# Performance work log

Hardware: AMD Instinct MI355X
Metric: run time of the kernel (lower is better)

The kernel has to match this reference:

```python
import jax, jax.numpy as jnp
import numpy as np

V, SMAX, D, L, H, F = 50257, 1024, 768, 12, 12, 3072
DH = D // H
SCALE = float(np.sqrt(DH))


def setup_inputs() -> dict:
    key = jax.random.key(0)
    ks = jax.random.split(key, 24)
    B, S = 2, 1024
    std = 0.02
    inp = {
        'input_ids': jax.random.randint(ks[0], (B, S), 0, V),
        'tok_emb': jax.random.normal(ks[1], (V, D), jnp.float32) * std,
        'pos_emb': jax.random.normal(ks[2], (SMAX, D), jnp.float32) * std,
        # stacked per-layer params (leading dim L)
        'Wq': jax.random.normal(ks[3], (L, D, D), jnp.float32) * std,
        'bq': jnp.zeros((L, D), jnp.float32),
        'Wk': jax.random.normal(ks[4], (L, D, D), jnp.float32) * std,
        'bk': jnp.zeros((L, D), jnp.float32),
        'Wv': jax.random.normal(ks[5], (L, D, D), jnp.float32) * std,
        'bv': jnp.zeros((L, D), jnp.float32),
        'Wo': jax.random.normal(ks[6], (L, D, D), jnp.float32) * std,
        'bo': jnp.zeros((L, D), jnp.float32),
        'ln1_g': jnp.ones((L, D), jnp.float32),
        'ln1_b': jnp.zeros((L, D), jnp.float32),
        'ln2_g': jnp.ones((L, D), jnp.float32),
        'ln2_b': jnp.zeros((L, D), jnp.float32),
        'W1': jax.random.normal(ks[7], (L, D, F), jnp.float32) * std,
        'b1': jnp.zeros((L, F), jnp.float32),
        'W2': jax.random.normal(ks[8], (L, F, D), jnp.float32) * std,
        'b2': jnp.zeros((L, D), jnp.float32),
        'lnf_g': jnp.ones((D,), jnp.float32),
        'lnf_b': jnp.zeros((D,), jnp.float32),
        'Whead': jax.random.normal(ks[9], (D, V), jnp.float32) * std,
    }
    return inp


def _layernorm(x, g, b, eps=1e-5):
    mu = jnp.mean(x, axis=-1, keepdims=True)
    var = jnp.var(x, axis=-1, keepdims=True)
    return (x - mu) * jax.lax.rsqrt(var + eps) * g + b


def _gpt_forward(input_ids, tok_emb, pos_emb, Wq, bq, Wk, bk, Wv, bv, Wo, bo,
                 ln1_g, ln1_b, ln2_g, ln2_b, W1, b1, W2, b2, lnf_g, lnf_b, Whead):
    B, S = input_ids.shape
    x = tok_emb[input_ids] + pos_emb[:S][None, :, :]  # (B,S,D)
    # additive causal mask: -inf above the diagonal
    idx = jnp.arange(S)
    neg_inf = jnp.finfo(x.dtype).min
    mask = jnp.where(idx[None, :] > idx[:, None], neg_inf, 0.0).astype(x.dtype)  # (S,S)

    def block(x, p):
        (wq, bq_, wk, bk_, wv, bv_, wo, bo_, g1, b1_, g2, b2_, w1, bb1, w2, bb2) = p
        h = _layernorm(x, g1, b1_)
        q = (h @ wq + bq_).reshape(B, S, H, DH)
        k = (h @ wk + bk_).reshape(B, S, H, DH)
        v = (h @ wv + bv_).reshape(B, S, H, DH)
        scores = jnp.einsum('bqhd,bkhd->bhqk', q, k) / SCALE + mask
        attn = jax.nn.softmax(scores, axis=-1)
        o = jnp.einsum('bhqk,bkhd->bqhd', attn, v).reshape(B, S, D)
        x = x + (o @ wo + bo_)
        h2 = _layernorm(x, g2, b2_)
        ffn = jax.nn.gelu(h2 @ w1 + bb1, approximate=False) @ w2 + bb2
        return x + ffn, None

    params = (Wq, bq, Wk, bk, Wv, bv, Wo, bo, ln1_g, ln1_b, ln2_g, ln2_b, W1, b1, W2, b2)
    x, _ = jax.lax.scan(block, x, params)
    x = _layernorm(x, lnf_g, lnf_b)
    return x @ Whead  # (B,S,V) logits


def reference(input_ids, tok_emb, pos_emb, Wq, bq, Wk, bk, Wv, bv, Wo, bo,
              ln1_g, ln1_b, ln2_g, ln2_b, W1, b1, W2, b2, lnf_g, lnf_b, Whead):
    return _gpt_forward(input_ids, tok_emb, pos_emb, Wq, bq, Wk, bk, Wv, bv, Wo, bo,
                        ln1_g, ln1_b, ln2_g, ln2_b, W1, b1, W2, b2, lnf_g, lnf_b, Whead)
```

## Files before the change

kernel.cpp:

```cpp
#include <hip/hip_runtime.h>
#include <hip/hip_bf16.h>
#include <cstdint>
#include <cstddef>

#define DEV __device__ __forceinline__

typedef __attribute__((ext_vector_type(8))) short short8;
typedef __attribute__((ext_vector_type(4))) short s16x4;
typedef __attribute__((ext_vector_type(4))) float f32x4;
typedef unsigned short u16;
typedef unsigned int u32;

static constexpr int Vv = 50257;
static constexpr int Dd = 768;
static constexpr int Ll = 12;
static constexpr int Hh = 12;
static constexpr int Ff = 3072;
static constexpr int Ss = 1024;
static constexpr int Bbatch = 2;
static constexpr int DHh = 64;
static constexpr int Mtok = Bbatch * Ss;
static constexpr int NQKV = 3 * Dd;
static constexpr int VPAD = 50304;

DEV u16 f2bf(float f){ u32 x; __builtin_memcpy(&x, &f, 4); x += 0x7fffu + ((x >> 16) & 1u); return (u16)(x >> 16); }

DEV void gld_lds16(const void* g, void* l){
  __builtin_amdgcn_global_load_lds((const __attribute__((address_space(1))) void*)g,
                                   (__attribute__((address_space(3))) void*)l, 16, 0, 0);
}

__global__ __launch_bounds__(256) void k_embed_ln(const int* __restrict__ ids, const float* __restrict__ tok,
                                                  const float* __restrict__ pos, const float* __restrict__ g,
                                                  const float* __restrict__ b, float* __restrict__ x,
                                                  u16* __restrict__ h){
  int t = blockIdx.x, tid = threadIdx.x;
  int id = ids[t];
  int s = t & (Ss - 1);
  const float* tr = tok + (size_t)id * Dd;
  const float* pr = pos + (size_t)s * Dd;
  float v0 = tr[tid] + pr[tid], v1 = tr[tid + 256] + pr[tid + 256], v2 = tr[tid + 512] + pr[tid + 512];
  float* xr = x + (size_t)t * Dd;
  xr[tid] = v0; xr[tid + 256] = v1; xr[tid + 512] = v2;
  float sm = v0 + v1 + v2, ss = v0 * v0 + v1 * v1 + v2 * v2;
  for (int o = 1; o < 64; o <<= 1){ sm += __shfl_xor(sm, o, 64); ss += __shfl_xor(ss, o, 64); }
  __shared__ float red[8];
  int w = tid >> 6, l = tid & 63;
  if (l == 0){ red[w] = sm; red[w + 4] = ss; }
  __syncthreads();
  sm = red[0] + red[1] + red[2] + red[3];
  ss = red[4] + red[5] + red[6] + red[7];
  float mu = sm * (1.0f / Dd);
  float var = ss * (1.0f / Dd) - mu * mu;
  float rs = rsqrtf(var + 1e-5f);
  u16* yr = h + (size_t)t * Dd;
  yr[tid]       = f2bf((v0 - mu) * rs * g[tid]       + b[tid]);
  yr[tid + 256] = f2bf((v1 - mu) * rs * g[tid + 256] + b[tid + 256]);
  yr[tid + 512] = f2bf((v2 - mu) * rs * g[tid + 512] + b[tid + 512]);
}

__global__ __launch_bounds__(256) void k_ln(const float* __restrict__ x, const float* __restrict__ g,
                                            const float* __restrict__ b, u16* __restrict__ y){
  int row = blockIdx.x, tid = threadIdx.x;
  const float* xr = x + (size_t)row * Dd;
  float v0 = xr[tid], v1 = xr[tid + 256], v2 = xr[tid + 512];
  float s = v0 + v1 + v2, ss = v0 * v0 + v1 * v1 + v2 * v2;
  for (int o = 1; o < 64; o <<= 1){ s += __shfl_xor(s, o, 64); ss += __shfl_xor(ss, o, 64); }
  __shared__ float red[8];
  int w = tid >> 6, l = tid & 63;
  if (l == 0){ red[w] = s; red[w + 4] = ss; }
  __syncthreads();
  s = red[0] + red[1] + red[2] + red[3];
  ss = red[4] + red[5] + red[6] + red[7];
  float mu = s * (1.0f / Dd);
  float var = ss * (1.0f / Dd) - mu * mu;
  float rs = rsqrtf(var + 1e-5f);
  u16* yr = y + (size_t)row * Dd;
  yr[tid]       = f2bf((v0 - mu) * rs * g[tid]       + b[tid]);
  yr[tid + 256] = f2bf((v1 - mu) * rs * g[tid + 256] + b[tid + 256]);
  yr[tid + 512] = f2bf((v2 - mu) * rs * g[tid + 512] + b[tid + 512]);
}

__global__ __launch_bounds__(256) void k_combineln(const float* __restrict__ p, const float* __restrict__ bias,
                                                   float* __restrict__ x, const float* __restrict__ g,
                                                   const float* __restrict__ b, u16* __restrict__ h){
  constexpr size_t SL = (size_t)Mtok * Dd;
  int row = blockIdx.x, tid = threadIdx.x;
  float* xr = x + (size_t)row * Dd;
  const float* p0 = p + (size_t)row * Dd;
  const float* p1 = p0 + SL;
  float v0 = xr[tid]       + p0[tid]       + p1[tid]       + bias[tid];
  float v1 = xr[tid + 256] + p0[tid + 256] + p1[tid + 256] + bias[tid + 256];
  float v2 = xr[tid + 512] + p0[tid + 512] + p1[tid + 512] + bias[tid + 512];
  xr[tid] = v0; xr[tid + 256] = v1; xr[tid + 512] = v2;
  float s = v0 + v1 + v2, ss = v0 * v0 + v1 * v1 + v2 * v2;
  for (int o = 1; o < 64; o <<= 1){ s += __shfl_xor(s, o, 64); ss += __shfl_xor(ss, o, 64); }
  __shared__ float red[8];
  int w = tid >> 6, l = tid & 63;
  if (l == 0){ red[w] = s; red[w + 4] = ss; }
  __syncthreads();
  s = red[0] + red[1] + red[2] + red[3];
  ss = red[4] + red[5] + red[6] + red[7];
  float mu = s * (1.0f / Dd);
  float var = ss * (1.0f / Dd) - mu * mu;
  float rs = rsqrtf(var + 1e-5f);
  u16* yr = h + (size_t)row * Dd;
  yr[tid]       = f2bf((v0 - mu) * rs * g[tid]       + b[tid]);
  yr[tid + 256] = f2bf((v1 - mu) * rs * g[tid + 256] + b[tid + 256]);
  yr[tid + 512] = f2bf((v2 - mu) * rs * g[tid + 512] + b[tid + 512]);
}

__global__ __launch_bounds__(256) void k_transpose(const float* __restrict__ src, u16* __restrict__ dst,
                                                   int R, int C, long smat, long dmat){
  __shared__ float tile[64][33];
  src += (size_t)blockIdx.z * smat;
  dst += (size_t)blockIdx.z * dmat;
  int c0 = blockIdx.x * 32, r0 = blockIdx.y * 64;
  int tid = threadIdx.x;
  int tc = tid & 31, tr = tid >> 5;
  #pragma unroll
  for (int i = 0; i < 8; i++){
    int r = tr + i * 8, c = c0 + tc;
    tile[r][tc] = (c < C) ? src[(size_t)(r0 + r) * C + c] : 0.0f;
  }
  __syncthreads();
  #pragma unroll
  for (int it = 0; it < 2; it++){
    int id = it * 256 + tid;
    int c = id & 31, rg = id >> 5, r = rg * 4;
    int cc = c0 + c;
    if (cc < C){
      s16x4 v = { (short)f2bf(tile[r][c]), (short)f2bf(tile[r + 1][c]),
                  (short)f2bf(tile[r + 2][c]), (short)f2bf(tile[r + 3][c]) };
      *(s16x4*)(dst + (size_t)cc * R + r0 + r) = v;
    }
  }
}

__global__ void k_biaspack(const float* __restrict__ bq, const float* __restrict__ bk,
                           const float* __restrict__ bv, float* __restrict__ o){
  int i = blockIdx.x * 256 + threadIdx.x;
  int col = i % NQKV, lay = i / NQKV;
  float v = (col < Dd) ? bq[lay * Dd + col]
          : (col < 2 * Dd) ? bk[lay * Dd + col - Dd]
          : bv[lay * Dd + col - 2 * Dd];
  o[i] = v;
}

template<int BM, int BN, int EPI>
__global__ __launch_bounds__(256) void k_gemmF(const u16* __restrict__ A, const u16* __restrict__ Bt,
    const float* __restrict__ bias, float* __restrict__ Cf, u16* __restrict__ Cb,
    u16* __restrict__ vt, int Nn, int MT, int NT){
  constexpr bool SPLIT = (EPI == 4);
  constexpr int KST  = SPLIT ? Ff : Dd;
  constexpr int KLEN = SPLIT ? (Ff / 2) : Dd;
  constexpr int nk = KLEN / 32;
  constexpr int HM = BM / 2, HN = BN / 2, FM = HM / 16, FN = HN / 16;
  constexpr int nA = (BM * 4) / 256, nB = (BN * 4) / 256;
  constexpr int ABYTE = BM * 64, BBYTE = BN * 64;
  __shared__ __align__(16) u16 ldsA[2 * BM * 32];
  __shared__ __align__(16) u16 ldsB[2 * BN * 32];
  int tid = threadIdx.x, wid = tid >> 6, l = tid & 63;
  int wm = wid >> 1, wn = wid & 1;
  int lr = l & 15, lc = l >> 4;
  int nwg = gridDim.x, dIdx = blockIdx.x;
  int L = (dIdx & 7) * (nwg >> 3) + (dIdx >> 3);
  int kidx = 0;
  if (SPLIT){ int per = MT * NT; kidx = L / per; L -= kidx * per; }
  int mtile = L % MT, ntile = L / MT;
  int m0 = mtile * BM, n0 = ntile * BN;
  int kbase = kidx * KLEN;

  const u16* gA[nA]; u16* dA[nA];
  const u16* gB[nB]; u16* dB[nB];
  #pragma unroll
  for (int i = 0; i < nA; i++){
    int id = i * 256 + tid, row = id >> 2, c = id & 3;
    int cs = c ^ ((row >> 1) & 3);
    gA[i] = A + (size_t)(m0 + row) * KST + kbase + cs * 8;
    dA[i] = ldsA + id * 8;
  }
  #pragma unroll
  for (int i = 0; i < nB; i++){
    int id = i * 256 + tid, row = id >> 2, c = id & 3;
    int cs = c ^ ((row >> 1) & 3);
    gB[i] = Bt + (size_t)(n0 + row) * KST + kbase + cs * 8;
    dB[i] = ldsB + id * 8;
  }
  int offA[FM], offB[FN];
  #pragma unroll
  for (int i = 0; i < FM; i++){
    int row = wm * HM + i * 16 + lr;
    offA[i] = row * 64 + ((lc ^ ((row >> 1) & 3)) << 4);
  }
  #pragma unroll
  for (int j = 0; j < FN; j++){
    int row = wn * HN + j * 16 + lr;
    offB[j] = row * 64 + ((lc ^ ((row >> 1) & 3)) << 4);
  }

  f32x4 acc[FM][FN];
  #pragma unroll
  for (int i = 0; i < FM; i++)
    #pragma unroll
    for (int j = 0; j < FN; j++) acc[i][j] = (f32x4)0.0f;

  auto stage = [&](int buf){
    #pragma unroll
    for (int i = 0; i < nA; i++){ gld_lds16(gA[i], (char*)dA[i] + buf * ABYTE); gA[i] += 32; }
    #pragma unroll
    for (int i = 0; i < nB; i++){ gld_lds16(gB[i], (char*)dB[i] + buf * BBYTE); gB[i] += 32; }
  };
  auto compute = [&](int buf){
    const char* bA = (const char*)ldsA + buf * ABYTE;
    const char* bB = (const char*)ldsB + buf * BBYTE;
    short8 af[FM], bfr[FN];
    #pragma unroll
    for (int i = 0; i < FM; i++) af[i] = *(const short8*)(bA + offA[i]);
    #pragma unroll
    for (int j = 0; j < FN; j++) bfr[j] = *(const short8*)(bB + offB[j]);
    #pragma unroll
    for (int i = 0; i < FM; i++)
      #pragma unroll
      for (int j = 0; j < FN; j++){
        if (EPI == 0)
          acc[i][j] = __builtin_amdgcn_mfma_f32_16x16x32_bf16(af[i], bfr[j], acc[i][j], 0, 0, 0);
        else
          acc[i][j] = __builtin_amdgcn_mfma_f32_16x16x32_bf16(bfr[j], af[i], acc[i][j], 0, 0, 0);
      }
  };

  stage(0);
  __syncthreads();
  #pragma unroll 1
  for (int t = 0; t < nk - 1; ++t){
    stage((t + 1) & 1);
    compute(t & 1);
    __syncthreads();
  }
  compute((nk - 1) & 1);

  if (EPI == 0){
    #pragma unroll
    for (int i = 0; i < FM; i++){
      #pragma unroll
      for (int j = 0; j < FN; j++){
        int col = n0 + wn * HN + j * 16 + lr;
        if (col >= Nn) continue;
        #pragma unroll
        for (int r = 0; r < 4; r++){
          int row = m0 + wm * HM + i * 16 + lc * 4 + r;
          Cf[(size_t)row * Nn + col] = acc[i][j][r];
        }
      }
    }
    return;
  }
  #pragma unroll
  for (int i = 0; i < FM; i++){
    int row = m0 + wm * HM + i * 16 + lr;
    #pragma unroll
    for (int j = 0; j < FN; j++){
      int c0 = n0 + wn * HN + j * 16 + lc * 4;
      f32x4 v = acc[i][j];
      if (EPI == 4){
        *(f32x4*)(Cf + (size_t)kidx * Mtok * Dd + (size_t)row * Dd + c0) = v;
        continue;
      }
      f32x4 bv = *(const f32x4*)(bias + c0);
      v = v + bv;
      if (EPI == 3){
        f32x4* p = (f32x4*)(Cf + (size_t)row * Nn + c0);
        *p = *p + v;
        continue;
      }
      if (EPI == 1 && c0 < Dd) v = v * 0.125f;
      if (EPI == 2){
        #pragma unroll
        for (int r = 0; r < 4; r++) v[r] = 0.5f * v[r] * (1.0f + erff(v[r] * 0.70710678118f));
      }
      u16 q0 = f2bf(v[0]), q1 = f2bf(v[1]), q2 = f2bf(v[2]), q3 = f2bf(v[3]);
      if (EPI == 1 && c0 >= 2 * Dd){
        int c2 = c0 - 2 * Dd, hh = c2 >> 6, dd2 = c2 & 63;
        int bb = row >> 10, ss2 = row & 1023;
        size_t base = ((size_t)((bb * Hh + hh) * DHh + dd2)) << 10;
        vt[base + ss2] = q0;
        vt[base + (1 << 10) + ss2] = q1;
        vt[base + (2 << 10) + ss2] = q2;
        vt[base + (3 << 10) + ss2] = q3;
      } else {
        s16x4 pv = { (short)q0, (short)q1, (short)q2, (short)q3 };
        *(s16x4*)(Cb + (size_t)row * Nn + c0) = pv;
      }
    }
  }
}

__global__ __launch_bounds__(256) void k_attn(const u16* __restrict__ qkv, const u16* __restrict__ vt,
                                              u16* __restrict__ o){
  __shared__ __align__(16) u16 ldsK[64 * 64];
  __shared__ __align__(16) u16 ldsV[64 * 64];
  __shared__ __align__(16) u16 ldsP[4][16 * 72];
  int bid = blockIdx.x;
  int iq = (Ss / 64) - 1 - (bid / (Bbatch * Hh));
  int bh = bid % (Bbatch * Hh);
  int b = bh / Hh, h = bh % Hh;
  int tid = threadIdx.x, wid = tid >> 6, l = tid & 63, lr = l & 15, lc = l >> 4;
  int nt = iq + 1;
  int qrow = b * Ss + iq * 64 + wid * 16 + lr;
  const u16* qp = qkv + (size_t)qrow * NQKV + h * DHh;
  short8 qf0 = *(const short8*)(qp + lc * 8);
  short8 qf1 = *(const short8*)(qp + 32 + lc * 8);

  const u16* gK[2]; const u16* gV[2]; u16* dK[2]; u16* dV[2];
  #pragma unroll
  for (int c = 0; c < 2; c++){
    int id = c * 256 + tid, row = id >> 3, ch = id & 7;
    int cs = ch ^ (row & 7);
    gK[c] = qkv + (size_t)(b * Ss + row) * NQKV + Dd + h * DHh + cs * 8;
    gV[c] = vt + ((size_t)(bh * DHh) + row) * Ss + cs * 8;
    dK[c] = ldsK + id * 8;
    dV[c] = ldsV + id * 8;
  }
  int koff[4][2];
  #pragma unroll
  for (int fn = 0; fn < 4; fn++){
    int kv = fn * 16 + lr;
    #pragma unroll
    for (int ks = 0; ks < 2; ks++){
      int ch = ks * 4 + lc;
      koff[fn][ks] = kv * 128 + ((ch ^ (kv & 7)) << 4);
    }
  }

  float mreg = -1e30f, lsum = 0.0f;
  f32x4 oacc[4];
  #pragma unroll
  for (int i = 0; i < 4; i++) oacc[i] = (f32x4)0.0f;
  u16* pbase = ldsP[wid];

  #pragma unroll 1
  for (int t = 0; t < nt; ++t){
    #pragma unroll
    for (int c = 0; c < 2; c++){ gld_lds16(gK[c], dK[c]); gK[c] += (size_t)64 * NQKV; }
    #pragma unroll
    for (int c = 0; c < 2; c++){ gld_lds16(gV[c], dV[c]); gV[c] += 64; }
    __syncthreads();
    f32x4 sc[4];
    __builtin_amdgcn_s_setprio(1);
    #pragma unroll
    for (int fn = 0; fn < 4; fn++){
      short8 kf0 = *(const short8*)((const char*)ldsK + koff[fn][0]);
      short8 kf1 = *(const short8*)((const char*)ldsK + koff[fn][1]);
      sc[fn] = __builtin_amdgcn_mfma_f32_16x16x32_bf16(kf0, qf0, (f32x4)0.0f, 0, 0, 0);
      sc[fn] = __builtin_amdgcn_mfma_f32_16x16x32_bf16(kf1, qf1, sc[fn], 0, 0, 0);
    }
    __builtin_amdgcn_s_setprio(0);
    if (t == iq){
      #pragma unroll
      for (int fn = 0; fn < 4; fn++)
        #pragma unroll
        for (int r = 0; r < 4; r++)
          if (fn * 16 + lc * 4 + r > wid * 16 + lr) sc[fn][r] = -1e30f;
    }
    float pm = sc[0][0];
    #pragma unroll
    for (int fn = 0; fn < 4; fn++)
      #pragma unroll
      for (int r = 0; r < 4; r++) pm = fmaxf(pm, sc[fn][r]);
    pm = fmaxf(pm, __shfl_xor(pm, 16, 64));
    pm = fmaxf(pm, __shfl_xor(pm, 32, 64));
    float mnew = fmaxf(mreg, pm);
    float alpha = __expf(mreg - mnew);
    mreg = mnew;
    float rs = 0.0f;
    #pragma unroll
    for (int fn = 0; fn < 4; fn++)
      #pragma unroll
      for (int r = 0; r < 4; r++){
        float p = __expf(sc[fn][r] - mnew);
        sc[fn][r] = p;
        rs += p;
      }
    rs += __shfl_xor(rs, 16, 64);
    rs += __shfl_xor(rs, 32, 64);
    lsum = lsum * alpha + rs;
    #pragma unroll
    for (int fn = 0; fn < 4; fn++){
      s16x4 pv = { (short)f2bf(sc[fn][0]), (short)f2bf(sc[fn][1]),
                   (short)f2bf(sc[fn][2]), (short)f2bf(sc[fn][3]) };
      *(s16x4*)((char*)pbase + lr * 144 + fn * 32 + lc * 8) = pv;
    }
    asm volatile("s_waitcnt lgkmcnt(0)" ::: "memory");
    __builtin_amdgcn_sched_barrier(0);
    #pragma unroll
    for (int fd = 0; fd < 4; fd++)
      #pragma unroll
      for (int r = 0; r < 4; r++) oacc[fd][r] *= alpha;
    short8 pa0 = *(const short8*)((const char*)pbase + lr * 144 + lc * 16);
    short8 pa1 = *(const short8*)((const char*)pbase + lr * 144 + 64 + lc * 16);
    __builtin_amdgcn_s_setprio(1);
    #pragma unroll
    for (int fd = 0; fd < 4; fd++){
      short8 vf0 = *(const short8*)((const char*)ldsV + koff[fd][0]);
      short8 vf1 = *(const short8*)((const char*)ldsV + koff[fd][1]);
      oacc[fd] = __builtin_amdgcn_mfma_f32_16x16x32_bf16(vf0, pa0, oacc[fd], 0, 0, 0);
      oacc[fd] = __builtin_amdgcn_mfma_f32_16x16x32_bf16(vf1, pa1, oacc[fd], 0, 0, 0);
    }
    __builtin_amdgcn_s_setprio(0);
    __syncthreads();
  }
  float inv = 1.0f / lsum;
  int rowg = b * Ss + iq * 64 + wid * 16 + lr;
  #pragma unroll
  for (int fd = 0; fd < 4; fd++){
    s16x4 ov = { (short)f2bf(oacc[fd][0] * inv), (short)f2bf(oacc[fd][1] * inv),
                 (short)f2bf(oacc[fd][2] * inv), (short)f2bf(oacc[fd][3] * inv) };
    *(s16x4*)(o + (size_t)rowg * Dd + h * DHh + fd * 16 + lc * 4) = ov;
  }
}

extern "C" void kernel_launch(void* const* d_in, const int* in_sizes, int n_in,
                              void* d_out, int out_size, void* d_ws, size_t ws_size,
                              hipStream_t stream){
  const int*   ids  = (const int*)d_in[0];
  const float* tok  = (const float*)d_in[1];
  const float* pos  = (const float*)d_in[2];
  const float* Wq   = (const float*)d_in[3];
  const float* bq   = (const float*)d_in[4];
  const float* Wk   = (const float*)d_in[5];
  const float* bk   = (const float*)d_in[6];
  const float* Wv   = (const float*)d_in[7];
  const float* bv   = (const float*)d_in[8];
  const float* Wo   = (const float*)d_in[9];
  const float* bo   = (const float*)d_in[10];
  const float* ln1g = (const float*)d_in[11];
  const float* ln1b = (const float*)d_in[12];
  const float* ln2g = (const float*)d_in[13];
  const float* ln2b = (const float*)d_in[14];
  const float* W1   = (const float*)d_in[15];
  const float* b1   = (const float*)d_in[16];
  const float* W2   = (const float*)d_in[17];
  const float* b2   = (const float*)d_in[18];
  const float* lnfg = (const float*)d_in[19];
  const float* lnfb = (const float*)d_in[20];
  const float* Wh   = (const float*)d_in[21];
  float* out = (float*)d_out;

  auto al = [](size_t x){ return (x + 255) & ~(size_t)255; };
  size_t off = 0;
  auto take = [&](size_t bytes){ size_t r = off; off = al(off + bytes); return r; };
  size_t o_x    = take((size_t)Mtok * Dd * 4);
  size_t o_h    = take((size_t)Mtok * Dd * 2);
  size_t o_qkv  = take((size_t)Mtok * NQKV * 2);
  size_t o_vt   = take((size_t)Bbatch * Hh * DHh * Ss * 2);
  size_t o_o    = take((size_t)Mtok * Dd * 2);
  size_t o_mid  = take((size_t)Mtok * Ff * 2);
  size_t o_bq   = take((size_t)Ll * NQKV * 4);
  size_t o_part = take((size_t)2 * Mtok * Dd * 4);
  size_t o_rot = off;
  size_t o_wqkv, o_wo, o_w1, o_w2, o_wh;
  bool full;
  {
    size_t t = off;
    o_wqkv = t; t = al(t + (size_t)Ll * NQKV * Dd * 2);
    o_wo   = t; t = al(t + (size_t)Ll * Dd * Dd * 2);
    o_w1   = t; t = al(t + (size_t)Ll * Ff * Dd * 2);
    o_w2   = t; t = al(t + (size_t)Ll * Dd * Ff * 2);
    o_wh   = t; t = al(t + (size_t)VPAD * Dd * 2);
    full = (t <= ws_size);
  }
  char* ws = (char*)d_ws;
  float* x    = (float*)(ws + o_x);
  u16*   h    = (u16*)(ws + o_h);
  u16*   qkvb = (u16*)(ws + o_qkv);
  u16*   vtb  = (u16*)(ws + o_vt);
  u16*   ob   = (u16*)(ws + o_o);
  u16*   midb = (u16*)(ws + o_mid);
  float* bqkvp= (float*)(ws + o_bq);
  float* part = (float*)(ws + o_part);
  u16* wqkvT = full ? (u16*)(ws + o_wqkv) : (u16*)(ws + o_rot);
  u16* woT   = full ? (u16*)(ws + o_wo)   : (u16*)(ws + o_rot);
  u16* w1T   = full ? (u16*)(ws + o_w1)   : (u16*)(ws + o_rot);
  u16* w2T   = full ? (u16*)(ws + o_w2)   : (u16*)(ws + o_rot);
  u16* whT   = full ? (u16*)(ws + o_wh)   : (u16*)(ws + o_rot);

  auto tpose = [&](const float* src, u16* dst, int R, int C, int nmat, long smat, long dmat){
    k_transpose<<<dim3((C + 31) / 32, R / 64, nmat), 256, 0, stream>>>(src, dst, R, C, smat, dmat);
  };

  k_biaspack<<<(Ll * NQKV) / 256, 256, 0, stream>>>(bq, bk, bv, bqkvp);
  k_embed_ln<<<Mtok, 256, 0, stream>>>(ids, tok, pos, ln1g, ln1b, x, h);

  if (full){
    tpose(Wq, wqkvT,              Dd, Dd, Ll, (long)Dd * Dd, (long)NQKV * Dd);
    tpose(Wk, wqkvT + Dd * Dd,    Dd, Dd, Ll, (long)Dd * Dd, (long)NQKV * Dd);
    tpose(Wv, wqkvT + 2 * Dd * Dd,Dd, Dd, Ll, (long)Dd * Dd, (long)NQKV * Dd);
    tpose(Wo, woT, Dd, Dd, Ll, (long)Dd * Dd, (long)Dd * Dd);
    tpose(W1, w1T, Dd, Ff, Ll, (long)Dd * Ff, (long)Ff * Dd);
    tpose(W2, w2T, Ff, Dd, Ll, (long)Ff * Dd, (long)Dd * Ff);
    tpose(Wh, whT, Dd, Vv, 1, 0, 0);
  }

  auto gemm_qkv = [&](const u16* Aop, const u16* Bop, const float* bias, u16* Cb){
    constexpr int MT = Mtok / 64, NT = NQKV / 128;
    k_gemmF<64, 128, 1><<<MT * NT, 256, 0, stream>>>(Aop, Bop, bias, nullptr, Cb, vtb, NQKV, MT, NT);
  };
  auto gemm_wo = [&](const u16* Aop, const u16* Bop, const float* bias, float* C){
    constexpr int MT = Mtok / 64, NT = Dd / 64;
    k_gemmF<64, 64, 3><<<MT * NT, 256, 0, stream>>>(Aop, Bop, bias, C, nullptr, nullptr, Dd, MT, NT);
  };
  auto gemm_ffn1 = [&](const u16* Aop, const u16* Bop, const float* bias, u16* Cb){
    constexpr int MT = Mtok / 64, NT = Ff / 128;
    k_gemmF<64, 128, 2><<<MT * NT, 256, 0, stream>>>(Aop, Bop, bias, nullptr, Cb, nullptr, Ff, MT, NT);
  };
  auto gemm_ffn2 = [&](const u16* Aop, const u16* Bop){
    constexpr int MT = Mtok / 64, NT = Dd / 64;
    k_gemmF<64, 64, 4><<<MT * NT * 2, 256, 0, stream>>>(Aop, Bop, nullptr, part, nullptr, nullptr, Dd, MT, NT);
  };
  auto gemm_head = [&](const u16* Aop, const u16* Bop, float* C){
    constexpr int MT = Mtok / 128, NT = VPAD / 128;
    k_gemmF<128, 128, 0><<<MT * NT, 256, 0, stream>>>(Aop, Bop, nullptr, C, nullptr, nullptr, Vv, MT, NT);
  };

  for (int l = 0; l < Ll; ++l){
    const u16* wqkvL = full ? wqkvT + (size_t)l * NQKV * Dd : wqkvT;
    const u16* woL   = full ? woT   + (size_t)l * Dd * Dd   : woT;
    const u16* w1L   = full ? w1T   + (size_t)l * Ff * Dd   : w1T;
    const u16* w2L   = full ? w2T   + (size_t)l * Dd * Ff   : w2T;
    if (!full){
      tpose(Wq + (size_t)l * Dd * Dd, wqkvT,              Dd, Dd, 1, 0, 0);
      tpose(Wk + (size_t)l * Dd * Dd, wqkvT + Dd * Dd,    Dd, Dd, 1, 0, 0);
      tpose(Wv + (size_t)l * Dd * Dd, wqkvT + 2 * Dd * Dd,Dd, Dd, 1, 0, 0);
    }
    gemm_qkv(h, wqkvL, bqkvp + l * NQKV, qkvb);
    k_attn<<<(Ss / 64) * Bbatch * Hh, 256, 0, stream>>>(qkvb, vtb, ob);
    if (!full) tpose(Wo + (size_t)l * Dd * Dd, woT, Dd, Dd, 1, 0, 0);
    gemm_wo(ob, woL, bo + l * Dd, x);
    k_ln<<<Mtok, 256, 0, stream>>>(x, ln2g + l * Dd, ln2b + l * Dd, h);
    if (!full) tpose(W1 + (size_t)l * Dd * Ff, w1T, Dd, Ff, 1, 0, 0);
    gemm_ffn1(h, w1L, b1 + l * Ff, midb);
    if (!full) tpose(W2 + (size_t)l * Ff * Dd, w2T, Ff, Dd, 1, 0, 0);
    gemm_ffn2(midb, w2L);
    const float* gN = (l + 1 < Ll) ? (ln1g + (l + 1) * Dd) : lnfg;
    const float* bN = (l + 1 < Ll) ? (ln1b + (l + 1) * Dd) : lnfb;
    k_combineln<<<Mtok, 256, 0, stream>>>(part, b2 + l * Dd, x, gN, bN, h);
  }
  if (!full) tpose(Wh, whT, Dd, Vv, 1, 0, 0);
  gemm_head(h, whT, out);
}
```

Before: 2.133 ms.

## Deepen GEMM pipeline to four LDS stages with explicit vmcnt waits

Replaces the double-buffered GEMM main loop with a four-slot LDS ring that keeps three global-to-LDS loads in flight, gated by explicit s_waitcnt vmcnt counts and raw barriers instead of __syncthreads. It also raises wave priority around the MFMA block and uses nontemporal stores for the large logits output. The aim is to hide global-load latency and cut barrier stalls. The cost is double the LDS per block, which can lower occupancy. The unrolled loop assumes the K-step count fits the 4-stage schedule, which holds for these shapes.

```diff
diff --git a/kernel.cpp b/kernel.cpp
--- a/kernel.cpp
+++ b/kernel.cpp
@@ -28,6 +28,19 @@
 DEV void gld_lds16(const void* g, void* l){
   __builtin_amdgcn_global_load_lds((const __attribute__((address_space(1))) void*)g,
                                    (__attribute__((address_space(3))) void*)l, 16, 0, 0);
+}
+
+template<int N> DEV void waitv(){
+  if constexpr (N == 0) asm volatile("s_waitcnt vmcnt(0)" ::: "memory");
+  else if constexpr (N == 2) asm volatile("s_waitcnt vmcnt(2)" ::: "memory");
+  else if constexpr (N == 3) asm volatile("s_waitcnt vmcnt(3)" ::: "memory");
+  else if constexpr (N == 4) asm volatile("s_waitcnt vmcnt(4)" ::: "memory");
+  else if constexpr (N == 6) asm volatile("s_waitcnt vmcnt(6)" ::: "memory");
+  else if constexpr (N == 8) asm volatile("s_waitcnt vmcnt(8)" ::: "memory");
+}
+DEV void barrier_sb(){
+  __builtin_amdgcn_s_barrier();
+  __builtin_amdgcn_sched_barrier(0);
 }
 
 __global__ __launch_bounds__(256) void k_embed_ln(const int* __restrict__ ids, const float* __restrict__ tok,
@@ -148,7 +161,7 @@
 }
 
 template<int BM, int BN, int EPI>
-__global__ __launch_bounds__(256) void k_gemmF(const u16* __restrict__ A, const u16* __restrict__ Bt,
+__global__ __launch_bounds__(256) void k_gemmR(const u16* __restrict__ A, const u16* __restrict__ Bt,
     const float* __restrict__ bias, float* __restrict__ Cf, u16* __restrict__ Cb,
     u16* __restrict__ vt, int Nn, int MT, int NT){
   constexpr bool SPLIT = (EPI == 4);
@@ -156,10 +169,10 @@
   constexpr int KLEN = SPLIT ? (Ff / 2) : Dd;
   constexpr int nk = KLEN / 32;
   constexpr int HM = BM / 2, HN = BN / 2, FM = HM / 16, FN = HN / 16;
-  constexpr int nA = (BM * 4) / 256, nB = (BN * 4) / 256;
+  constexpr int nA = (BM * 4) / 256, nB = (BN * 4) / 256, NL = nA + nB;
   constexpr int ABYTE = BM * 64, BBYTE = BN * 64;
-  __shared__ __align__(16) u16 ldsA[2 * BM * 32];
-  __shared__ __align__(16) u16 ldsB[2 * BN * 32];
+  __shared__ __align__(16) u16 ldsA[4 * BM * 32];
+  __shared__ __align__(16) u16 ldsB[4 * BN * 32];
   int tid = threadIdx.x, wid = tid >> 6, l = tid & 63;
   int wm = wid >> 1, wn = wid & 1;
   int lr = l & 15, lc = l >> 4;
@@ -205,20 +218,23 @@
     #pragma unroll
     for (int j = 0; j < FN; j++) acc[i][j] = (f32x4)0.0f;
 
-  auto stage = [&](int buf){
-    #pragma unroll
-    for (int i = 0; i < nA; i++){ gld_lds16(gA[i], (char*)dA[i] + buf * ABYTE); gA[i] += 32; }
-    #pragma unroll
-    for (int i = 0; i < nB; i++){ gld_lds16(gB[i], (char*)dB[i] + buf * BBYTE); gB[i] += 32; }
-  };
-  auto compute = [&](int buf){
-    const char* bA = (const char*)ldsA + buf * ABYTE;
-    const char* bB = (const char*)ldsB + buf * BBYTE;
+  auto stage = [&](int slot){
+    #pragma unroll
+    for (int i = 0; i < nA; i++){ gld_lds16(gA[i], (char*)dA[i] + slot * ABYTE); gA[i] += 32; }
+    #pragma unroll
+    for (int i = 0; i < nB; i++){ gld_lds16(gB[i], (char*)dB[i] + slot * BBYTE); gB[i] += 32; }
+  };
+  auto compute = [&](int slot){
+    const char* bA = (const char*)ldsA + slot * ABYTE;
+    const char* bB = (const char*)ldsB + slot * BBYTE;
     short8 af[FM], bfr[FN];
     #pragma unroll
     for (int i = 0; i < FM; i++) af[i] = *(const short8*)(bA + offA[i]);
     #pragma unroll
     for (int j = 0; j < FN; j++) bfr[j] = *(const short8*)(bB + offB[j]);
+    asm volatile("s_waitcnt lgkmcnt(0)" ::: "memory");
+    __builtin_amdgcn_sched_barrier(0);
+    __builtin_amdgcn_s_setprio(1);
     #pragma unroll
     for (int i = 0; i < FM; i++)
       #pragma unroll
@@ -228,17 +244,22 @@
         else
           acc[i][j] = __builtin_amdgcn_mfma_f32_16x16x32_bf16(bfr[j], af[i], acc[i][j], 0, 0, 0);
       }
-  };
-
-  stage(0);
-  __syncthreads();
+    __builtin_amdgcn_s_setprio(0);
+  };
+
+  stage(0); stage(1); stage(2);
+  waitv<2 * NL>(); barrier_sb();
   #pragma unroll 1
-  for (int t = 0; t < nk - 1; ++t){
-    stage((t + 1) & 1);
-    compute(t & 1);
-    __syncthreads();
-  }
-  compute((nk - 1) & 1);
+  for (int it = 0; it < (nk - 4) / 4; ++it){
+    stage(3); compute(0); waitv<2 * NL>(); barrier_sb();
+    stage(0); compute(1); waitv<2 * NL>(); barrier_sb();
+    stage(1); compute(2); waitv<2 * NL>(); barrier_sb();
+    stage(2); compute(3); waitv<2 * NL>(); barrier_sb();
+  }
+  stage(3); compute(0); waitv<2 * NL>(); barrier_sb();
+  compute(1); waitv<NL>(); barrier_sb();
+  compute(2); waitv<0>(); barrier_sb();
+  compute(3);
 
   if (EPI == 0){
     #pragma unroll
@@ -250,7 +271,7 @@
         #pragma unroll
         for (int r = 0; r < 4; r++){
           int row = m0 + wm * HM + i * 16 + lc * 4 + r;
-          Cf[(size_t)row * Nn + col] = acc[i][j][r];
+          __builtin_nontemporal_store(acc[i][j][r], &Cf[(size_t)row * Nn + col]);
         }
       }
     }
@@ -504,23 +525,23 @@
 
   auto gemm_qkv = [&](const u16* Aop, const u16* Bop, const float* bias, u16* Cb){
     constexpr int MT = Mtok / 64, NT = NQKV / 128;
-    k_gemmF<64, 128, 1><<<MT * NT, 256, 0, stream>>>(Aop, Bop, bias, nullptr, Cb, vtb, NQKV, MT, NT);
+    k_gemmR<64, 128, 1><<<MT * NT, 256, 0, stream>>>(Aop, Bop, bias, nullptr, Cb, vtb, NQKV, MT, NT);
   };
   auto gemm_wo = [&](const u16* Aop, const u16* Bop, const float* bias, float* C){
     constexpr int MT = Mtok / 64, NT = Dd / 64;
-    k_gemmF<64, 64, 3><<<MT * NT, 256, 0, stream>>>(Aop, Bop, bias, C, nullptr, nullptr, Dd, MT, NT);
+    k_gemmR<64, 64, 3><<<MT * NT, 256, 0, stream>>>(Aop, Bop, bias, C, nullptr, nullptr, Dd, MT, NT);
   };
   auto gemm_ffn1 = [&](const u16* Aop, const u16* Bop, const float* bias, u16* Cb){
     constexpr int MT = Mtok / 64, NT = Ff / 128;
-    k_gemmF<64, 128, 2><<<MT * NT, 256, 0, stream>>>(Aop, Bop, bias, nullptr, Cb, nullptr, Ff, MT, NT);
+    k_gemmR<64, 128, 2><<<MT * NT, 256, 0, stream>>>(Aop, Bop, bias, nullptr, Cb, nullptr, Ff, MT, NT);
   };
   auto gemm_ffn2 = [&](const u16* Aop, const u16* Bop){
     constexpr int MT = Mtok / 64, NT = Dd / 64;
-    k_gemmF<64, 64, 4><<<MT * NT * 2, 256, 0, stream>>>(Aop, Bop, nullptr, part, nullptr, nullptr, Dd, MT, NT);
+    k_gemmR<64, 64, 4><<<MT * NT * 2, 256, 0, stream>>>(Aop, Bop, nullptr, part, nullptr, nullptr, Dd, MT, NT);
   };
   auto gemm_head = [&](const u16* Aop, const u16* Bop, float* C){
     constexpr int MT = Mtok / 128, NT = VPAD / 128;
-    k_gemmF<128, 128, 0><<<MT * NT, 256, 0, stream>>>(Aop, Bop, nullptr, C, nullptr, nullptr, Vv, MT, NT);
+    k_gemmR<128, 128, 0><<<MT * NT, 256, 0, stream>>>(Aop, Bop, nullptr, C, nullptr, nullptr, Vv, MT, NT);
   };
 
   for (int l = 0; l < Ll; ++l){
```

Result: slower. 2.225 ms (+4.3%).
